# Performance work log

Measured on AMD Instinct MI355X. Metric: run time of the kernel, lower is better.

The kernel has to match this reference:

```python
import jax, jax.numpy as jnp
import numpy as np

N_NODES = 50000
N_EDGES = 800000
IN_C = 128
HID_C = 2 * IN_C  # 256
OUT_C = 128
NEG_SLOPE = 0.2


def _gat_layer(x, edge_src, edge_dst, W, a_src, a_dst, b, n_nodes):
    # x: [N, Fin], W: [Fin, Fout], a_src/a_dst: [Fout], b: [Fout]
    h = x @ W                                   # [N, Fout]
    alpha_src = h @ a_src                       # [N]
    alpha_dst = h @ a_dst                       # [N]
    e = alpha_src[edge_src] + alpha_dst[edge_dst]           # [E]
    e = jnp.where(e > 0, e, NEG_SLOPE * e)      # LeakyReLU(0.2)
    # segment softmax over incoming edges of each destination node
    m = jax.ops.segment_max(e, edge_dst, num_segments=n_nodes)  # [N]
    w = jnp.exp(e - m[edge_dst])                               # [E]
    z = jax.ops.segment_sum(w, edge_dst, num_segments=n_nodes)  # [N]
    alpha = w / z[edge_dst]                                     # [E]
    # scatter-aggregate messages
    out = jax.ops.segment_sum(alpha[:, None] * h[edge_src], edge_dst,
                              num_segments=n_nodes)             # [N, Fout]
    return out + b


def setup_inputs() -> dict:
    key = jax.random.key(0)
    ks = jax.random.split(key, 12)
    x = jax.random.normal(ks[0], (N_NODES, IN_C), dtype=jnp.float32)
    edge_index = jax.random.randint(ks[1], (2, N_EDGES), 0, N_NODES, dtype=jnp.int32)
    def glorot(k, shape):
        fan_in = shape[0] if len(shape) == 2 else shape[0]
        return jax.random.normal(k, shape, dtype=jnp.float32) / np.sqrt(fan_in)
    W1 = glorot(ks[2], (IN_C, HID_C))
    a1_src = glorot(ks[3], (HID_C,))
    a1_dst = glorot(ks[4], (HID_C,))
    b1 = jnp.zeros((HID_C,), dtype=jnp.float32)
    W2 = glorot(ks[5], (HID_C, OUT_C))
    a2_src = glorot(ks[6], (OUT_C,))
    a2_dst = glorot(ks[7], (OUT_C,))
    b2 = jnp.zeros((OUT_C,), dtype=jnp.float32)
    return {"x": x, "edge_index": edge_index, "W1": W1, "a1_src": a1_src,
            "a1_dst": a1_dst, "b1": b1, "W2": W2, "a2_src": a2_src,
            "a2_dst": a2_dst, "b2": b2}


def reference(x, edge_index, W1, a1_src, a1_dst, b1, W2, a2_src, a2_dst, b2):
    n = x.shape[0]
    # PyG GATConv default: add self-loops
    loops = jnp.arange(n, dtype=edge_index.dtype)
    src = jnp.concatenate([edge_index[0], loops])
    dst = jnp.concatenate([edge_index[1], loops])
    h = _gat_layer(x, src, dst, W1, a1_src, a1_dst, b1, n)
    h = jax.nn.relu(h)
    out = _gat_layer(h, src, dst, W2, a2_src, a2_dst, b2, n)
    return out
```

## Files before the change

### kernel.cpp

```cpp
#include <hip/hip_runtime.h>
#include <hip/hip_bf16.h>
#include <math.h>

#define N_NODES 50000
#define N_EDGESX 800000
#define E_TOT   (N_EDGESX + N_NODES)
#define IN_C 128
#define HID_C 256
#define OUT_C 128
#define NEG_SLOPE 0.2f

#define NPB   100
#define NBUCK ((N_NODES + NPB - 1) / NPB)
#define BCAP  2560
#define EPB   4096
#define NABLK ((E_TOT + EPB - 1) / EPB)

typedef __attribute__((ext_vector_type(8))) short short8;
typedef __attribute__((ext_vector_type(4))) float floatx4;
typedef __attribute__((ext_vector_type(2))) float floatx2;

__device__ __forceinline__ float bf2f(short s) {
    unsigned u = ((unsigned)(unsigned short)s) << 16;
    float f; __builtin_memcpy(&f, &u, 4); return f;
}
__device__ __forceinline__ short f2bf(float f) {
    unsigned u; __builtin_memcpy(&u, &f, 4);
    unsigned r = (u + 0x7FFFu + ((u >> 16) & 1u)) >> 16;
    return (short)r;
}

template<int KROWS, int NCOLS>
__global__ __launch_bounds__(256)
void gemv_p_kernel(const float* __restrict__ W, const float* __restrict__ a_s,
                   const float* __restrict__ a_d, float* __restrict__ ps, float* __restrict__ pd) {
    int t = threadIdx.x;
    int k = t & (KROWS - 1);
    const float* av = (t < KROWS) ? a_s : a_d;
    float* pv = (t < KROWS) ? ps : pd;
    const float* row = W + (size_t)k * NCOLS;
    float s = 0.f;
    for (int n = 0; n < NCOLS; ++n) s += row[n] * av[n];
    pv[k] = s;
}

__global__ __launch_bounds__(256)
void alpha_x_kernel(const float* __restrict__ x, const float* __restrict__ ps,
                    const float* __restrict__ pd, float* __restrict__ as_out,
                    float* __restrict__ ad_out, short* __restrict__ xb) {
    int gt = blockIdx.x * blockDim.x + threadIdx.x;
    int node = gt >> 6, lane = gt & 63;
    if (node >= N_NODES) return;
    floatx2 xv = *(const floatx2*)&x[(size_t)node * IN_C + lane * 2];
    floatx2 s2 = *(const floatx2*)&ps[lane * 2];
    floatx2 d2 = *(const floatx2*)&pd[lane * 2];
    float s = xv[0] * s2[0] + xv[1] * s2[1];
    float d = xv[0] * d2[0] + xv[1] * d2[1];
    unsigned pack = (unsigned)(unsigned short)f2bf(xv[0]) | ((unsigned)(unsigned short)f2bf(xv[1]) << 16);
    *(unsigned*)&xb[(size_t)node * IN_C + lane * 2] = pack;
    #pragma unroll
    for (int off = 32; off; off >>= 1) {
        s += __shfl_down(s, off);
        d += __shfl_down(d, off);
    }
    if (lane == 0) { as_out[node] = s; ad_out[node] = d; }
}

__global__ __launch_bounds__(256)
void binA_kernel(const int* __restrict__ src, const int* __restrict__ dst,
                 int* __restrict__ bcnt, int2* __restrict__ stage) {
    __shared__ int hist[NBUCK];
    __shared__ int base[NBUCK];
    for (int b = threadIdx.x; b < NBUCK; b += 256) hist[b] = 0;
    __syncthreads();
    int e0 = blockIdx.x * EPB;
    int e1 = min(e0 + EPB, E_TOT);
    for (int i = e0 + threadIdx.x; i < e1; i += 256) {
        int d = (i < N_EDGESX) ? dst[i] : (i - N_EDGESX);
        atomicAdd(&hist[d / NPB], 1);
    }
    __syncthreads();
    for (int b = threadIdx.x; b < NBUCK; b += 256) {
        int c = hist[b];
        base[b] = c ? atomicAdd(&bcnt[b], c) : 0;
        hist[b] = 0;
    }
    __syncthreads();
    for (int i = e0 + threadIdx.x; i < e1; i += 256) {
        int s, d;
        if (i < N_EDGESX) { s = src[i]; d = dst[i]; }
        else { s = i - N_EDGESX; d = s; }
        int b = d / NPB;
        int off = base[b] + atomicAdd(&hist[b], 1);
        if (off < BCAP) stage[(size_t)b * BCAP + off] = make_int2(s, d);
    }
}

__global__ __launch_bounds__(128)
void bucket_count_kernel(const int* __restrict__ bcnt, const int2* __restrict__ stage,
                         int* __restrict__ cnt) {
    __shared__ int lc[NPB];
    int b = blockIdx.x;
    for (int t = threadIdx.x; t < NPB; t += 128) lc[t] = 0;
    __syncthreads();
    int n = min(bcnt[b], BCAP);
    const int2* sp = stage + (size_t)b * BCAP;
    for (int i = threadIdx.x; i < n; i += 128)
        atomicAdd(&lc[sp[i].y - b * NPB], 1);
    __syncthreads();
    int nb = b * NPB;
    for (int t = threadIdx.x; t < NPB; t += 128)
        if (nb + t < N_NODES) cnt[nb + t] = lc[t];
}

__global__ __launch_bounds__(128)
void bucket_scatter_kernel(const int* __restrict__ bcnt, const int2* __restrict__ stage,
                           const int* __restrict__ row_ptr, const float* __restrict__ as_in,
                           const float* __restrict__ ad_in, int* __restrict__ esrc,
                           float* __restrict__ ew) {
    __shared__ int cur[NPB];
    __shared__ float adl[NPB];
    int b = blockIdx.x;
    int nb = b * NPB;
    for (int t = threadIdx.x; t < NPB; t += 128) {
        int node = nb + t;
        cur[t] = (node < N_NODES) ? row_ptr[node] : 0;
        adl[t] = (node < N_NODES) ? ad_in[node] : 0.f;
    }
    __syncthreads();
    int n = min(bcnt[b], BCAP);
    const int2* sp = stage + (size_t)b * BCAP;
    for (int i = threadIdx.x; i < n; i += 128) {
        int2 e = sp[i];
        int li = e.y - nb;
        int pos = atomicAdd(&cur[li], 1);
        esrc[pos] = e.x;
        float v = as_in[e.x] + adl[li];
        ew[pos] = v > 0.f ? v : NEG_SLOPE * v;
    }
}

#define NBLK ((N_NODES + 1023) / 1024)

__global__ __launch_bounds__(1024)
void scan_a_kernel(const int* __restrict__ cnt, int* __restrict__ row_ptr, int* __restrict__ bsum) {
    __shared__ int buf[1024];
    int tid = threadIdx.x;
    int idx = blockIdx.x * 1024 + tid;
    int v = (idx < N_NODES) ? cnt[idx] : 0;
    buf[tid] = v;
    __syncthreads();
    for (int off = 1; off < 1024; off <<= 1) {
        int t = (tid >= off) ? buf[tid - off] : 0;
        __syncthreads();
        buf[tid] += t;
        __syncthreads();
    }
    if (idx < N_NODES) row_ptr[idx] = buf[tid] - v;
    if (tid == 1023) bsum[blockIdx.x] = buf[1023];
}

__global__ void scan_b_kernel(int* __restrict__ bsum, int* __restrict__ row_ptr) {
    int lane = threadIdx.x;
    int v = (lane < NBLK) ? bsum[lane] : 0;
    int s = v;
    #pragma unroll
    for (int off = 1; off < 64; off <<= 1) {
        int t = __shfl_up(s, off);
        if (lane >= off) s += t;
    }
    if (lane < NBLK) bsum[lane] = s - v;
    if (lane == 63) row_ptr[N_NODES] = s;
}

__global__ __launch_bounds__(1024)
void scan_c_kernel(int* __restrict__ row_ptr, const int* __restrict__ bsum) {
    int idx = blockIdx.x * 1024 + threadIdx.x;
    if (idx < N_NODES) row_ptr[idx] += bsum[blockIdx.x];
}

__global__ __launch_bounds__(256)
void fill_edst_kernel(const int* __restrict__ row_ptr, int* __restrict__ edst) {
    int gt = blockIdx.x * blockDim.x + threadIdx.x;
    int node = gt >> 6, lane = gt & 63;
    if (node >= N_NODES) return;
    int beg = row_ptr[node], end = row_ptr[node + 1];
    for (int i = beg + lane; i < end; i += 64) edst[i] = node;
}

__global__ void ew_kernel(const int* __restrict__ esrc, const int* __restrict__ edst,
                          const float* __restrict__ as_in, const float* __restrict__ ad_in,
                          float* __restrict__ ew) {
    int i = blockIdx.x * blockDim.x + threadIdx.x;
    if (i >= E_TOT) return;
    float e = as_in[esrc[i]] + ad_in[edst[i]];
    ew[i] = e > 0.f ? e : NEG_SLOPE * e;
}

__global__ void splitT_kernel(const float* __restrict__ W, short* __restrict__ th,
                              short* __restrict__ tl, int K, int N) {
    int i = blockIdx.x * blockDim.x + threadIdx.x;
    if (i >= K * N) return;
    int k = i / N, n = i - k * N;
    float f = W[i];
    short hb = f2bf(f);
    th[n * K + k] = hb;
    tl[n * K + k] = f2bf(f - bf2f(hb));
}

template<int K, int OUTMODE>
__global__ __launch_bounds__(256)
void gemm_mfma(const short* __restrict__ Ah, const short* __restrict__ Al,
               const short* __restrict__ Bth, const short* __restrict__ Btl,
               int N, const float* __restrict__ bias,
               short* __restrict__ C0, short* __restrict__ C1) {
    __shared__ short Ah_s[128][40];
    __shared__ short Al_s[128][40];
    __shared__ short Bh_s[64][40];
    __shared__ short Bl_s[64][40];
    int tid = threadIdx.x;
    int lane = tid & 63, wave = tid >> 6;
    int wr = wave >> 1, wc = wave & 1;
    int bm = blockIdx.y * 128, bn = blockIdx.x * 64;
    int l15 = lane & 15, kf = (lane >> 4) * 8;

    floatx4 acc[4][2];
    #pragma unroll
    for (int i = 0; i < 4; ++i)
        #pragma unroll
        for (int j = 0; j < 2; ++j) acc[i][j] = (floatx4){0.f, 0.f, 0.f, 0.f};

    int arow = tid >> 1, ac0 = (tid & 1) * 16;
    int brow = tid >> 2, bc0 = (tid & 3) * 8;
    int agm = bm + arow;
    bool aval = agm < N_NODES;

    for (int k0 = 0; k0 < K; k0 += 32) {
        short8 va0 = {0,0,0,0,0,0,0,0}, va1 = va0, vl0 = va0, vl1 = va0;
        if (aval) {
            const short* pa = Ah + (size_t)agm * K + k0 + ac0;
            va0 = *(const short8*)pa; va1 = *(const short8*)(pa + 8);
            const short* pl = Al + (size_t)agm * K + k0 + ac0;
            vl0 = *(const short8*)pl; vl1 = *(const short8*)(pl + 8);
        }
        *(short8*)&Ah_s[arow][ac0]     = va0;
        *(short8*)&Ah_s[arow][ac0 + 8] = va1;
        *(short8*)&Al_s[arow][ac0]     = vl0;
        *(short8*)&Al_s[arow][ac0 + 8] = vl1;
        {
            const short* pb = Bth + (size_t)(bn + brow) * K + k0 + bc0;
            *(short8*)&Bh_s[brow][bc0] = *(const short8*)pb;
            const short* pb2 = Btl + (size_t)(bn + brow) * K + k0 + bc0;
            *(short8*)&Bl_s[brow][bc0] = *(const short8*)pb2;
        }
        __syncthreads();
        short8 afh[4], afl[4], bfh[2], bfl[2];
        #pragma unroll
        for (int mr = 0; mr < 4; ++mr) {
            int r = wr * 64 + mr * 16 + l15;
            afh[mr] = *(const short8*)&Ah_s[r][kf];
            afl[mr] = *(const short8*)&Al_s[r][kf];
        }
        #pragma unroll
        for (int nr = 0; nr < 2; ++nr) {
            int c = wc * 32 + nr * 16 + l15;
            bfh[nr] = *(const short8*)&Bh_s[c][kf];
            bfl[nr] = *(const short8*)&Bl_s[c][kf];
        }
        #pragma unroll
        for (int mr = 0; mr < 4; ++mr)
            #pragma unroll
            for (int nr = 0; nr < 2; ++nr) {
                acc[mr][nr] = __builtin_amdgcn_mfma_f32_16x16x32_bf16(afh[mr], bfh[nr], acc[mr][nr], 0, 0, 0);
                acc[mr][nr] = __builtin_amdgcn_mfma_f32_16x16x32_bf16(afh[mr], bfl[nr], acc[mr][nr], 0, 0, 0);
                acc[mr][nr] = __builtin_amdgcn_mfma_f32_16x16x32_bf16(afl[mr], bfh[nr], acc[mr][nr], 0, 0, 0);
            }
        __syncthreads();
    }
    float bv[2];
    if (OUTMODE == 2) {
        #pragma unroll
        for (int nr = 0; nr < 2; ++nr) bv[nr] = bias[bn + wc * 32 + nr * 16 + l15];
    }
    #pragma unroll
    for (int mr = 0; mr < 4; ++mr) {
        #pragma unroll
        for (int reg = 0; reg < 4; ++reg) {
            int gr = bm + wr * 64 + mr * 16 + (lane >> 4) * 4 + reg;
            if (gr < N_NODES) {
                #pragma unroll
                for (int nr = 0; nr < 2; ++nr) {
                    int gc = bn + wc * 32 + nr * 16 + l15;
                    float v = acc[mr][nr][reg];
                    if (OUTMODE == 1) {
                        C0[(size_t)gr * N + gc] = f2bf(v);
                    } else {
                        v = fmaxf(v + bv[nr], 0.f);
                        short hb = f2bf(v);
                        C0[(size_t)gr * N + gc] = hb;
                        C1[(size_t)gr * N + gc] = f2bf(v - bf2f(hb));
                    }
                }
            }
        }
    }
}

__global__ __launch_bounds__(256)
void alpha_bf16_128(const short* __restrict__ h, const float* __restrict__ a_src,
                    const float* __restrict__ a_dst, float* __restrict__ as_out,
                    float* __restrict__ ad_out) {
    int gt = blockIdx.x * blockDim.x + threadIdx.x;
    int node = gt >> 6, lane = gt & 63;
    if (node >= N_NODES) return;
    unsigned u = *(const unsigned*)&h[(size_t)node * OUT_C + lane * 2];
    float v0 = bf2f((short)(u & 0xFFFFu));
    float v1 = bf2f((short)(u >> 16));
    floatx2 as2 = *(const floatx2*)&a_src[lane * 2];
    floatx2 ad2 = *(const floatx2*)&a_dst[lane * 2];
    float s = v0 * as2[0] + v1 * as2[1];
    float d = v0 * ad2[0] + v1 * ad2[1];
    #pragma unroll
    for (int off = 32; off; off >>= 1) {
        s += __shfl_down(s, off);
        d += __shfl_down(d, off);
    }
    if (lane == 0) { as_out[node] = s; ad_out[node] = d; }
}

template<int OUT>
__global__ __launch_bounds__(256)
void aggregate_kernel(const short* __restrict__ h, const float* __restrict__ ew,
                      const int* __restrict__ row_ptr, const int* __restrict__ esrc,
                      const float* __restrict__ bias,
                      short* __restrict__ o_hi, short* __restrict__ o_lo,
                      float* __restrict__ o_f32) {
    int gt = blockIdx.x * blockDim.x + threadIdx.x;
    int node = gt >> 6, lane = gt & 63;
    if (node >= N_NODES) return;
    int beg = row_ptr[node], end = row_ptr[node + 1];

    float ml = -1e30f, zl = 0.f;
    for (int i = beg + lane; i < end; i += 64) {
        float e = ew[i];
        float mn = fmaxf(ml, e);
        zl = zl * __expf(ml - mn) + __expf(e - mn);
        ml = mn;
    }
    #pragma unroll
    for (int off = 32; off; off >>= 1) {
        float mo = __shfl_xor(ml, off);
        float zo = __shfl_xor(zl, off);
        float mn = fmaxf(ml, mo);
        zl = zl * __expf(ml - mn) + zo * __expf(mo - mn);
        ml = mn;
    }
    float m = ml;
    float inv_z = 1.f / zl;

    int grp = lane >> 4, l = lane & 15;
    float acc[8] = {};
    int i = beg;
    for (; i + 4 < end; i += 8) {
        int e0 = i + grp;
        int e1 = i + 4 + grp;
        bool v1 = e1 < end;
        int s0 = esrc[e0];
        int s1 = esrc[v1 ? e1 : beg];
        float w0 = __expf(ew[e0] - m) * inv_z;
        float w1 = v1 ? __expf(ew[e1] - m) * inv_z : 0.f;
        short8 hv0 = *(const short8*)&h[(size_t)s0 * 128 + l * 8];
        short8 hv1 = *(const short8*)&h[(size_t)s1 * 128 + l * 8];
        #pragma unroll
        for (int j = 0; j < 8; ++j) acc[j] += w0 * bf2f(hv0[j]);
        #pragma unroll
        for (int j = 0; j < 8; ++j) acc[j] += w1 * bf2f(hv1[j]);
    }
    if (i < end) {
        int e = i + grp;
        bool v = e < end;
        int s = esrc[v ? e : beg];
        float w = v ? __expf(ew[e] - m) * inv_z : 0.f;
        short8 hv = *(const short8*)&h[(size_t)s * 128 + l * 8];
        #pragma unroll
        for (int j = 0; j < 8; ++j) acc[j] += w * bf2f(hv[j]);
    }
    #pragma unroll
    for (int j = 0; j < 8; ++j) {
        acc[j] += __shfl_xor(acc[j], 16);
        acc[j] += __shfl_xor(acc[j], 32);
    }

    if (lane < 16) {
        if (OUT == 0) {
            short8 oh, ol;
            #pragma unroll
            for (int j = 0; j < 8; ++j) {
                short hb = f2bf(acc[j]);
                oh[j] = hb;
                ol[j] = f2bf(acc[j] - bf2f(hb));
            }
            *(short8*)&o_hi[(size_t)node * 128 + l * 8] = oh;
            *(short8*)&o_lo[(size_t)node * 128 + l * 8] = ol;
        } else {
            const float* brow = &bias[l * 8];
            floatx4 o0, o1;
            #pragma unroll
            for (int j = 0; j < 4; ++j) {
                o0[j] = acc[j] + brow[j];
                o1[j] = acc[j + 4] + brow[j + 4];
            }
            float* orow = &o_f32[(size_t)node * 128 + l * 8];
            *(floatx4*)orow = o0;
            *(floatx4*)(orow + 4) = o1;
        }
    }
}

extern "C" void kernel_launch(void* const* d_in, const int* in_sizes, int n_in,
                              void* d_out, int out_size, void* d_ws, size_t ws_size,
                              hipStream_t stream) {
    const float* x   = (const float*)d_in[0];
    const int*   ei  = (const int*)d_in[1];
    const float* W1  = (const float*)d_in[2];
    const float* a1s = (const float*)d_in[3];
    const float* a1d = (const float*)d_in[4];
    const float* b1  = (const float*)d_in[5];
    const float* W2  = (const float*)d_in[6];
    const float* a2s = (const float*)d_in[7];
    const float* a2d = (const float*)d_in[8];
    const float* b2  = (const float*)d_in[9];
    float* out = (float*)d_out;

    const int* e_src = ei;
    const int* e_dst = ei + N_EDGESX;

    char* ws = (char*)d_ws;
    const size_t OFF_XB    = 0;
    const size_t OFF_UH    = 12800000;
    const size_t OFF_UL    = 25600000;
    const size_t OFF_G1H   = 38400000;
    const size_t OFF_G1L   = 64000000;
    const size_t OFF_H2    = 89600000;
    const size_t OFF_W1TH  = 102400000;
    const size_t OFF_W1TL  = 102465536;
    const size_t OFF_W2TH  = 102531072;
    const size_t OFF_W2TL  = 102596608;
    const size_t OFF_P1S   = 102662144;
    const size_t OFF_P1D   = 102662656;
    const size_t OFF_AS    = 102663168;
    const size_t OFF_AD    = 102863360;
    const size_t OFF_RP    = 103063552;
    const size_t OFF_CNT   = 103264000;
    const size_t OFF_BSUM  = 103464192;
    const size_t OFF_BCNT  = 103464448;
    const size_t OFF_ESRC  = 103466496;
    const size_t OFF_EDST  = 106866496;
    const size_t OFF_EW    = 110266496;
    const size_t OFF_STAGE = 113666496;

    short* xb   = (short*)(ws + OFF_XB);
    short* uh   = (short*)(ws + OFF_UH);
    short* ul   = (short*)(ws + OFF_UL);
    short* g1h  = (short*)(ws + OFF_G1H);
    short* g1l  = (short*)(ws + OFF_G1L);
    short* h2   = (short*)(ws + OFF_H2);
    short* w1th = (short*)(ws + OFF_W1TH);
    short* w1tl = (short*)(ws + OFF_W1TL);
    short* w2th = (short*)(ws + OFF_W2TH);
    short* w2tl = (short*)(ws + OFF_W2TL);
    float* p1s  = (float*)(ws + OFF_P1S);
    float* p1d  = (float*)(ws + OFF_P1D);
    float* as_b = (float*)(ws + OFF_AS);
    float* ad_b = (float*)(ws + OFF_AD);
    int* row_ptr = (int*)(ws + OFF_RP);
    int* cnt     = (int*)(ws + OFF_CNT);
    int* bsum    = (int*)(ws + OFF_BSUM);
    int* bcnt    = (int*)(ws + OFF_BCNT);
    int* esrc    = (int*)(ws + OFF_ESRC);
    int* edst    = (int*)(ws + OFF_EDST);
    float* ewb   = (float*)(ws + OFF_EW);
    int2* stage  = (int2*)(ws + OFF_STAGE);

    int egrid = (E_TOT + 255) / 256;
    int ngrid = (N_NODES * 64 + 255) / 256;

    gemv_p_kernel<IN_C, HID_C><<<1, 256, 0, stream>>>(W1, a1s, a1d, p1s, p1d);
    alpha_x_kernel<<<ngrid, 256, 0, stream>>>(x, p1s, p1d, as_b, ad_b, xb);

    hipMemsetAsync(bcnt, 0, NBUCK * sizeof(int), stream);
    binA_kernel<<<NABLK, 256, 0, stream>>>(e_src, e_dst, bcnt, stage);
    bucket_count_kernel<<<NBUCK, 128, 0, stream>>>(bcnt, stage, cnt);
    scan_a_kernel<<<NBLK, 1024, 0, stream>>>(cnt, row_ptr, bsum);
    scan_b_kernel<<<1, 64, 0, stream>>>(bsum, row_ptr);
    scan_c_kernel<<<NBLK, 1024, 0, stream>>>(row_ptr, bsum);
    bucket_scatter_kernel<<<NBUCK, 128, 0, stream>>>(bcnt, stage, row_ptr, as_b, ad_b, esrc, ewb);
    fill_edst_kernel<<<ngrid, 256, 0, stream>>>(row_ptr, edst);

    splitT_kernel<<<(IN_C * HID_C + 255) / 256, 256, 0, stream>>>(W1, w1th, w1tl, IN_C, HID_C);
    splitT_kernel<<<(HID_C * OUT_C + 255) / 256, 256, 0, stream>>>(W2, w2th, w2tl, HID_C, OUT_C);

    aggregate_kernel<0><<<ngrid, 256, 0, stream>>>(xb, ewb, row_ptr, esrc, nullptr, uh, ul, nullptr);
    gemm_mfma<IN_C, 2><<<dim3(HID_C / 64, (N_NODES + 127) / 128), 256, 0, stream>>>(
        uh, ul, w1th, w1tl, HID_C, b1, g1h, g1l);

    gemm_mfma<HID_C, 1><<<dim3(OUT_C / 64, (N_NODES + 127) / 128), 256, 0, stream>>>(
        g1h, g1l, w2th, w2tl, OUT_C, nullptr, h2, nullptr);
    alpha_bf16_128<<<ngrid, 256, 0, stream>>>(h2, a2s, a2d, as_b, ad_b);
    ew_kernel<<<egrid, 256, 0, stream>>>(esrc, edst, as_b, ad_b, ewb);
    aggregate_kernel<1><<<ngrid, 256, 0, stream>>>(h2, ewb, row_ptr, esrc, b2, nullptr, nullptr, out);
}
```

Baseline: 309.2 us.

## Drop low-bf16 split of hidden activations, pack staged edges, unroll gather

The second GEMM now takes only the high bf16 half of the hidden activations. This removes the low-half store from GEMM1, the low-half loads in GEMM2 and one of its three MFMAs per tile, which lowers precision of the hidden layer. Staged edges are packed into one int (local dst in the high bits, src in the low 17 bits), halving stage traffic. The aggregate gather loop is unrolled to four edges per group per iteration to keep more loads in flight.

```diff
diff --git a/kernel.cpp b/kernel.cpp
--- a/kernel.cpp
+++ b/kernel.cpp
@@ -68,7 +68,7 @@
 
 __global__ __launch_bounds__(256)
 void binA_kernel(const int* __restrict__ src, const int* __restrict__ dst,
-                 int* __restrict__ bcnt, int2* __restrict__ stage) {
+                 int* __restrict__ bcnt, int* __restrict__ stage) {
     __shared__ int hist[NBUCK];
     __shared__ int base[NBUCK];
     for (int b = threadIdx.x; b < NBUCK; b += 256) hist[b] = 0;
@@ -92,21 +92,21 @@
         else { s = i - N_EDGESX; d = s; }
         int b = d / NPB;
         int off = base[b] + atomicAdd(&hist[b], 1);
-        if (off < BCAP) stage[(size_t)b * BCAP + off] = make_int2(s, d);
+        if (off < BCAP) stage[(size_t)b * BCAP + off] = ((d - b * NPB) << 17) | s;
     }
 }
 
 __global__ __launch_bounds__(128)
-void bucket_count_kernel(const int* __restrict__ bcnt, const int2* __restrict__ stage,
+void bucket_count_kernel(const int* __restrict__ bcnt, const int* __restrict__ stage,
                          int* __restrict__ cnt) {
     __shared__ int lc[NPB];
     int b = blockIdx.x;
     for (int t = threadIdx.x; t < NPB; t += 128) lc[t] = 0;
     __syncthreads();
     int n = min(bcnt[b], BCAP);
-    const int2* sp = stage + (size_t)b * BCAP;
+    const int* sp = stage + (size_t)b * BCAP;
     for (int i = threadIdx.x; i < n; i += 128)
-        atomicAdd(&lc[sp[i].y - b * NPB], 1);
+        atomicAdd(&lc[sp[i] >> 17], 1);
     __syncthreads();
     int nb = b * NPB;
     for (int t = threadIdx.x; t < NPB; t += 128)
@@ -114,7 +114,7 @@
 }
 
 __global__ __launch_bounds__(128)
-void bucket_scatter_kernel(const int* __restrict__ bcnt, const int2* __restrict__ stage,
+void bucket_scatter_kernel(const int* __restrict__ bcnt, const int* __restrict__ stage,
                            const int* __restrict__ row_ptr, const float* __restrict__ as_in,
                            const float* __restrict__ ad_in, int* __restrict__ esrc,
                            float* __restrict__ ew) {
@@ -129,14 +129,15 @@
     }
     __syncthreads();
     int n = min(bcnt[b], BCAP);
-    const int2* sp = stage + (size_t)b * BCAP;
+    const int* sp = stage + (size_t)b * BCAP;
     for (int i = threadIdx.x; i < n; i += 128) {
-        int2 e = sp[i];
-        int li = e.y - nb;
+        int v = sp[i];
+        int s = v & 0x1FFFF;
+        int li = v >> 17;
         int pos = atomicAdd(&cur[li], 1);
-        esrc[pos] = e.x;
-        float v = as_in[e.x] + adl[li];
-        ew[pos] = v > 0.f ? v : NEG_SLOPE * v;
+        esrc[pos] = s;
+        float e = as_in[s] + adl[li];
+        ew[pos] = e > 0.f ? e : NEG_SLOPE * e;
     }
 }
 
@@ -208,14 +209,13 @@
     tl[n * K + k] = f2bf(f - bf2f(hb));
 }
 
-template<int K, int OUTMODE>
+template<int K, int HASALO, int OUTMODE>
 __global__ __launch_bounds__(256)
 void gemm_mfma(const short* __restrict__ Ah, const short* __restrict__ Al,
                const short* __restrict__ Bth, const short* __restrict__ Btl,
-               int N, const float* __restrict__ bias,
-               short* __restrict__ C0, short* __restrict__ C1) {
+               int N, const float* __restrict__ bias, short* __restrict__ C0) {
     __shared__ short Ah_s[128][40];
-    __shared__ short Al_s[128][40];
+    __shared__ short Al_s[HASALO ? 128 : 1][HASALO ? 40 : 1];
     __shared__ short Bh_s[64][40];
     __shared__ short Bl_s[64][40];
     int tid = threadIdx.x;
@@ -236,17 +236,22 @@
     bool aval = agm < N_NODES;
 
     for (int k0 = 0; k0 < K; k0 += 32) {
-        short8 va0 = {0,0,0,0,0,0,0,0}, va1 = va0, vl0 = va0, vl1 = va0;
+        short8 va0 = {0,0,0,0,0,0,0,0}, va1 = va0;
         if (aval) {
             const short* pa = Ah + (size_t)agm * K + k0 + ac0;
             va0 = *(const short8*)pa; va1 = *(const short8*)(pa + 8);
-            const short* pl = Al + (size_t)agm * K + k0 + ac0;
-            vl0 = *(const short8*)pl; vl1 = *(const short8*)(pl + 8);
         }
         *(short8*)&Ah_s[arow][ac0]     = va0;
         *(short8*)&Ah_s[arow][ac0 + 8] = va1;
-        *(short8*)&Al_s[arow][ac0]     = vl0;
-        *(short8*)&Al_s[arow][ac0 + 8] = vl1;
+        if (HASALO) {
+            short8 vl0 = {0,0,0,0,0,0,0,0}, vl1 = vl0;
+            if (aval) {
+                const short* pl = Al + (size_t)agm * K + k0 + ac0;
+                vl0 = *(const short8*)pl; vl1 = *(const short8*)(pl + 8);
+            }
+            *(short8*)&Al_s[arow][ac0]     = vl0;
+            *(short8*)&Al_s[arow][ac0 + 8] = vl1;
+        }
         {
             const short* pb = Bth + (size_t)(bn + brow) * K + k0 + bc0;
             *(short8*)&Bh_s[brow][bc0] = *(const short8*)pb;
@@ -254,12 +259,11 @@
             *(short8*)&Bl_s[brow][bc0] = *(const short8*)pb2;
         }
         __syncthreads();
-        short8 afh[4], afl[4], bfh[2], bfl[2];
+        short8 afh[4], bfh[2], bfl[2];
         #pragma unroll
         for (int mr = 0; mr < 4; ++mr) {
             int r = wr * 64 + mr * 16 + l15;
             afh[mr] = *(const short8*)&Ah_s[r][kf];
-            afl[mr] = *(const short8*)&Al_s[r][kf];
         }
         #pragma unroll
         for (int nr = 0; nr < 2; ++nr) {
@@ -273,8 +277,20 @@
             for (int nr = 0; nr < 2; ++nr) {
                 acc[mr][nr] = __builtin_amdgcn_mfma_f32_16x16x32_bf16(afh[mr], bfh[nr], acc[mr][nr], 0, 0, 0);
                 acc[mr][nr] = __builtin_amdgcn_mfma_f32_16x16x32_bf16(afh[mr], bfl[nr], acc[mr][nr], 0, 0, 0);
-                acc[mr][nr] = __builtin_amdgcn_mfma_f32_16x16x32_bf16(afl[mr], bfh[nr], acc[mr][nr], 0, 0, 0);
             }
+        if (HASALO) {
+            short8 afl[4];
+            #pragma unroll
+            for (int mr = 0; mr < 4; ++mr) {
+                int r = wr * 64 + mr * 16 + l15;
+                afl[mr] = *(const short8*)&Al_s[r][kf];
+            }
+            #pragma unroll
+            for (int mr = 0; mr < 4; ++mr)
+                #pragma unroll
+                for (int nr = 0; nr < 2; ++nr)
+                    acc[mr][nr] = __builtin_amdgcn_mfma_f32_16x16x32_bf16(afl[mr], bfh[nr], acc[mr][nr], 0, 0, 0);
+        }
         __syncthreads();
     }
     float bv[2];
@@ -292,14 +308,8 @@
                 for (int nr = 0; nr < 2; ++nr) {
                     int gc = bn + wc * 32 + nr * 16 + l15;
                     float v = acc[mr][nr][reg];
-                    if (OUTMODE == 1) {
-                        C0[(size_t)gr * N + gc] = f2bf(v);
-                    } else {
-                        v = fmaxf(v + bv[nr], 0.f);
-                        short hb = f2bf(v);
-                        C0[(size_t)gr * N + gc] = hb;
-                        C1[(size_t)gr * N + gc] = f2bf(v - bf2f(hb));
-                    }
+                    if (OUTMODE == 2) v = fmaxf(v + bv[nr], 0.f);
+                    C0[(size_t)gr * N + gc] = f2bf(v);
                 }
             }
         }
@@ -361,22 +371,27 @@
     int grp = lane >> 4, l = lane & 15;
     float acc[8] = {};
     int i = beg;
-    for (; i + 4 < end; i += 8) {
-        int e0 = i + grp;
-        int e1 = i + 4 + grp;
-        bool v1 = e1 < end;
-        int s0 = esrc[e0];
-        int s1 = esrc[v1 ? e1 : beg];
+    for (; i + 16 <= end; i += 16) {
+        int e0 = i + grp, e1 = e0 + 4, e2 = e0 + 8, e3 = e0 + 12;
+        int s0 = esrc[e0], s1 = esrc[e1], s2 = esrc[e2], s3 = esrc[e3];
         float w0 = __expf(ew[e0] - m) * inv_z;
-        float w1 = v1 ? __expf(ew[e1] - m) * inv_z : 0.f;
+        float w1 = __expf(ew[e1] - m) * inv_z;
+        float w2 = __expf(ew[e2] - m) * inv_z;
+        float w3 = __expf(ew[e3] - m) * inv_z;
         short8 hv0 = *(const short8*)&h[(size_t)s0 * 128 + l * 8];
         short8 hv1 = *(const short8*)&h[(size_t)s1 * 128 + l * 8];
+        short8 hv2 = *(const short8*)&h[(size_t)s2 * 128 + l * 8];
+        short8 hv3 = *(const short8*)&h[(size_t)s3 * 128 + l * 8];
         #pragma unroll
         for (int j = 0; j < 8; ++j) acc[j] += w0 * bf2f(hv0[j]);
         #pragma unroll
         for (int j = 0; j < 8; ++j) acc[j] += w1 * bf2f(hv1[j]);
-    }
-    if (i < end) {
+        #pragma unroll
+        for (int j = 0; j < 8; ++j) acc[j] += w2 * bf2f(hv2[j]);
+        #pragma unroll
+        for (int j = 0; j < 8; ++j) acc[j] += w3 * bf2f(hv3[j]);
+    }
+    for (; i < end; i += 4) {
         int e = i + grp;
         bool v = e < end;
         int s = esrc[v ? e : beg];
@@ -440,30 +455,28 @@
     const size_t OFF_UH    = 12800000;
     const size_t OFF_UL    = 25600000;
     const size_t OFF_G1H   = 38400000;
-    const size_t OFF_G1L   = 64000000;
-    const size_t OFF_H2    = 89600000;
-    const size_t OFF_W1TH  = 102400000;
-    const size_t OFF_W1TL  = 102465536;
-    const size_t OFF_W2TH  = 102531072;
-    const size_t OFF_W2TL  = 102596608;
-    const size_t OFF_P1S   = 102662144;
-    const size_t OFF_P1D   = 102662656;
-    const size_t OFF_AS    = 102663168;
-    const size_t OFF_AD    = 102863360;
-    const size_t OFF_RP    = 103063552;
-    const size_t OFF_CNT   = 103264000;
-    const size_t OFF_BSUM  = 103464192;
-    const size_t OFF_BCNT  = 103464448;
-    const size_t OFF_ESRC  = 103466496;
-    const size_t OFF_EDST  = 106866496;
-    const size_t OFF_EW    = 110266496;
-    const size_t OFF_STAGE = 113666496;
+    const size_t OFF_H2    = 64000000;
+    const size_t OFF_W1TH  = 76800000;
+    const size_t OFF_W1TL  = 76865536;
+    const size_t OFF_W2TH  = 76931072;
+    const size_t OFF_W2TL  = 76996608;
+    const size_t OFF_P1S   = 77062144;
+    const size_t OFF_P1D   = 77062656;
+    const size_t OFF_AS    = 77063168;
+    const size_t OFF_AD    = 77263360;
+    const size_t OFF_RP    = 77463552;
+    const size_t OFF_CNT   = 77664000;
+    const size_t OFF_BSUM  = 77864192;
+    const size_t OFF_BCNT  = 77864448;
+    const size_t OFF_ESRC  = 77866496;
+    const size_t OFF_EDST  = 81266496;
+    const size_t OFF_EW    = 84666496;
+    const size_t OFF_STAGE = 88066496;
 
     short* xb   = (short*)(ws + OFF_XB);
     short* uh   = (short*)(ws + OFF_UH);
     short* ul   = (short*)(ws + OFF_UL);
     short* g1h  = (short*)(ws + OFF_G1H);
-    short* g1l  = (short*)(ws + OFF_G1L);
     short* h2   = (short*)(ws + OFF_H2);
     short* w1th = (short*)(ws + OFF_W1TH);
     short* w1tl = (short*)(ws + OFF_W1TL);
@@ -480,7 +493,7 @@
     int* esrc    = (int*)(ws + OFF_ESRC);
     int* edst    = (int*)(ws + OFF_EDST);
     float* ewb   = (float*)(ws + OFF_EW);
-    int2* stage  = (int2*)(ws + OFF_STAGE);
+    int* stage   = (int*)(ws + OFF_STAGE);
 
     int egrid = (E_TOT + 255) / 256;
     int ngrid = (N_NODES * 64 + 255) / 256;
@@ -501,11 +514,11 @@
     splitT_kernel<<<(HID_C * OUT_C + 255) / 256, 256, 0, stream>>>(W2, w2th, w2tl, HID_C, OUT_C);
 
     aggregate_kernel<0><<<ngrid, 256, 0, stream>>>(xb, ewb, row_ptr, esrc, nullptr, uh, ul, nullptr);
-    gemm_mfma<IN_C, 2><<<dim3(HID_C / 64, (N_NODES + 127) / 128), 256, 0, stream>>>(
-        uh, ul, w1th, w1tl, HID_C, b1, g1h, g1l);
-
-    gemm_mfma<HID_C, 1><<<dim3(OUT_C / 64, (N_NODES + 127) / 128), 256, 0, stream>>>(
-        g1h, g1l, w2th, w2tl, OUT_C, nullptr, h2, nullptr);
+    gemm_mfma<IN_C, 1, 2><<<dim3(HID_C / 64, (N_NODES + 127) / 128), 256, 0, stream>>>(
+        uh, ul, w1th, w1tl, HID_C, b1, g1h);
+
+    gemm_mfma<HID_C, 0, 1><<<dim3(OUT_C / 64, (N_NODES + 127) / 128), 256, 0, stream>>>(
+        g1h, nullptr, w2th, w2tl, OUT_C, nullptr, h2);
     alpha_bf16_128<<<ngrid, 256, 0, stream>>>(h2, a2s, a2d, as_b, ad_b);
     ew_kernel<<<egrid, 256, 0, stream>>>(esrc, edst, as_b, ad_b, ewb);
     aggregate_kernel<1><<<ngrid, 256, 0, stream>>>(h2, ewb, row_ptr, esrc, b2, nullptr, nullptr, out);
```

Result: faster. 299.1 us (-3.3%).
